# Kernel tuning notes

Hardware: AMD Instinct MI355X
Metric: run time of the kernel (lower is better)

Reference implementation:

```python
import jax, jax.numpy as jnp
import numpy as np

E, E2, T, C, H = 500_000, 1_000_000, 1_000_000, 64, 64
EPS, EPS2 = 0.0, 0.0  # train_eps=False, eps=eps2=0.0


def setup_inputs() -> dict:
    key = jax.random.key(0)
    ks = jax.random.split(key, 16)
    s = 1.0 / np.sqrt(C)
    return {
        "edge_attr": jax.random.normal(ks[0], (E, C), jnp.float32),
        "edge_attr2": jax.random.normal(ks[1], (E2, C), jnp.float32),
        # 6 projection layers (C -> C)
        "Wp": jax.random.normal(ks[2], (6, C, C), jnp.float32) * s,
        "bp": jnp.zeros((6, C), jnp.float32),
        # MLP 0 (for 1-hop edges): C -> H -> C
        "W1a": jax.random.normal(ks[3], (C, H), jnp.float32) * s,
        "b1a": jnp.zeros((H,), jnp.float32),
        "W2a": jax.random.normal(ks[4], (H, C), jnp.float32) * (1.0 / np.sqrt(H)),
        "b2a": jnp.zeros((C,), jnp.float32),
        # MLP 1 (for 2-hop edges): C -> H -> C
        "W1b": jax.random.normal(ks[5], (C, H), jnp.float32) * s,
        "b1b": jnp.zeros((H,), jnp.float32),
        "W2b": jax.random.normal(ks[6], (H, C), jnp.float32) * (1.0 / np.sqrt(H)),
        "b2b": jnp.zeros((C,), jnp.float32),
        # triangle index lists [3, T]; all values < E so valid for both edge arrays
        "triangle_1_1_1": jax.random.randint(ks[7], (3, T), 0, E, jnp.int64),
        "triangle_1_1_2": jax.random.randint(ks[8], (3, T), 0, E, jnp.int64),
        "triangle_1_2_2": jax.random.randint(ks[9], (3, T), 0, E, jnp.int64),
        "triangle_2_2_2": jax.random.randint(ks[10], (3, T), 0, E, jnp.int64),
        "inverse_edge_1": jax.random.randint(ks[11], (E,), 0, E, jnp.int64),
        "inverse_edge_2": jax.random.randint(ks[12], (E2,), 0, E, jnp.int64),
    }


def reference(edge_attr, edge_attr2, Wp, bp, W1a, b1a, W2a, b2a,
              W1b, b1b, W2b, b2b,
              triangle_1_1_1, triangle_1_1_2, triangle_1_2_2, triangle_2_2_2,
              inverse_edge_1, inverse_edge_2):
    num_edges = edge_attr.shape[0]
    num_edges2 = edge_attr2.shape[0]

    def proj(i, x):  # Linear proj i applied to gathered-sum features
        return x @ Wp[i] + bp[i]

    def mlp_a(x):
        return jax.nn.relu(x @ W1a + b1a) @ W2a + b2a

    def mlp_b(x):
        return jax.nn.relu(x @ W1b + b1b) @ W2b + b2b

    ij111, ik111, kj111 = triangle_1_1_1
    ij112, ik112, kj112 = triangle_1_1_2
    ij122, ik122, kj122 = triangle_1_2_2
    ij222, ik222, kj222 = triangle_2_2_2

    m111 = jax.ops.segment_sum(proj(0, edge_attr[ik111] + edge_attr[kj111]), ij111, num_segments=num_edges)
    m112 = jax.ops.segment_sum(proj(1, edge_attr[ik112] + edge_attr2[kj112]), ij112, num_segments=num_edges)
    m122 = jax.ops.segment_sum(proj(2, edge_attr2[ik122] + edge_attr2[kj122]), ij122, num_segments=num_edges)
    edge_attr = mlp_a(edge_attr * (1.0 + EPS) + m111 + m112 + m112[inverse_edge_1] + m122)

    m211 = jax.ops.segment_sum(proj(3, edge_attr[ij112] + edge_attr[ik112]), kj112, num_segments=num_edges2)
    m212 = jax.ops.segment_sum(proj(4, edge_attr[ij122] + edge_attr2[kj122]), ik122, num_segments=num_edges2)
    m222 = jax.ops.segment_sum(proj(5, edge_attr2[ik222] + edge_attr2[kj222]), ij222, num_segments=num_edges2)
    edge_attr2 = mlp_b(edge_attr2 * (1.0 + EPS2) + m211 + m212 + m212[inverse_edge_2] + m222)

    return (edge_attr, edge_attr2)
```

## Files before the change

### kernel.cpp

```cpp
#include <hip/hip_runtime.h>

#define CH 64
typedef unsigned int uint;
typedef unsigned short ushort;

typedef __attribute__((ext_vector_type(8))) short bf16x8;
typedef __attribute__((ext_vector_type(4))) float f32x4;

__device__ __forceinline__ float bf_lo(uint u){ union{uint a;float f;}c; c.a=u<<16; return c.f; }
__device__ __forceinline__ float bf_hi(uint u){ union{uint a;float f;}c; c.a=u&0xffff0000u; return c.f; }
__device__ __forceinline__ ushort f2bf(float f){
    uint a = __float_as_uint(f);
    a = (a + 0x7fffu + ((a>>16)&1u)) >> 16;
    return (ushort)a;
}
__device__ __forceinline__ uint pack2(float lo, float hi){
    return (uint)f2bf(lo) | ((uint)f2bf(hi) << 16);
}
__device__ __forceinline__ void atom_pk(uint* addr, float lo, float hi){
    uint v = pack2(lo, hi);
    asm volatile("global_atomic_pk_add_bf16 %0, %1, off" :: "v"(addr), "v"(v));
}

template<bool ABF, bool BBF>
__global__ __launch_bounds__(256) void scatter_sum(
    const void* __restrict__ Av, const void* __restrict__ Bv,
    const int* __restrict__ idx_dst, const int* __restrict__ idx_a,
    const int* __restrict__ idx_b, int T,
    uint* __restrict__ S, float* __restrict__ cnt)
{
    const int l32  = threadIdx.x & 31;
    const int half = (threadIdx.x >> 5) & 1;
    const int wave  = blockIdx.x * (blockDim.x >> 6) + (threadIdx.x >> 6);
    const int nwave = gridDim.x * (blockDim.x >> 6);

    for (int w = wave; 4 * w < T; w += nwave) {
        const int t0 = 4 * w + half;
        const int t1 = t0 + 2;
        const bool v0 = t0 < T, v1 = t1 < T;
        const int u0 = v0 ? t0 : 0;
        const int u1 = v1 ? t1 : 0;
        const int ia0 = idx_a[u0], ib0 = idx_b[u0], id0 = idx_dst[u0];
        const int ia1 = idx_a[u1], ib1 = idx_b[u1], id1 = idx_dst[u1];

        float ax0, ay0, bx0, by0, ax1, ay1, bx1, by1;
        if (ABF) { uint u = ((const uint*)Av)[(size_t)ia0*32 + l32]; ax0 = bf_lo(u); ay0 = bf_hi(u); }
        else     { float2 v = ((const float2*)Av)[(size_t)ia0*32 + l32]; ax0 = v.x; ay0 = v.y; }
        if (BBF) { uint u = ((const uint*)Bv)[(size_t)ib0*32 + l32]; bx0 = bf_lo(u); by0 = bf_hi(u); }
        else     { float2 v = ((const float2*)Bv)[(size_t)ib0*32 + l32]; bx0 = v.x; by0 = v.y; }
        if (ABF) { uint u = ((const uint*)Av)[(size_t)ia1*32 + l32]; ax1 = bf_lo(u); ay1 = bf_hi(u); }
        else     { float2 v = ((const float2*)Av)[(size_t)ia1*32 + l32]; ax1 = v.x; ay1 = v.y; }
        if (BBF) { uint u = ((const uint*)Bv)[(size_t)ib1*32 + l32]; bx1 = bf_lo(u); by1 = bf_hi(u); }
        else     { float2 v = ((const float2*)Bv)[(size_t)ib1*32 + l32]; bx1 = v.x; by1 = v.y; }

        if (v0) {
            atom_pk(S + (size_t)id0*32 + l32, ax0+bx0, ay0+by0);
            if (l32 == 0) atomicAdd(&cnt[id0], 1.0f);
        }
        if (v1) {
            atom_pk(S + (size_t)id1*32 + l32, ax1+bx1, ay1+by1);
            if (l32 == 0) atomicAdd(&cnt[id1], 1.0f);
        }
    }
}

__global__ __launch_bounds__(256) void conv_bf16_kernel(
    const float* __restrict__ src, uint* __restrict__ dst, long n4)
{
    long i = (long)blockIdx.x * blockDim.x + threadIdx.x;
    const long stride = (long)gridDim.x * blockDim.x;
    for (; i < n4; i += stride) {
        const float4 v = ((const float4*)src)[i];
        uint2 o; o.x = pack2(v.x, v.y); o.y = pack2(v.z, v.w);
        ((uint2*)dst)[i] = o;
    }
}

__global__ __launch_bounds__(256) void fused_finalize_mfma(
    const float* __restrict__ base,
    const uint* __restrict__ SA, const float* __restrict__ cA,
    const float* __restrict__ WA, const float* __restrict__ bA,
    const uint* __restrict__ SB, const float* __restrict__ cB,
    const float* __restrict__ WB, const float* __restrict__ bB,
    const uint* __restrict__ SC, const float* __restrict__ cC,
    const float* __restrict__ WC, const float* __restrict__ bC,
    const int* __restrict__ inv,
    const float* __restrict__ W1, const float* __restrict__ b1,
    const float* __restrict__ W2, const float* __restrict__ b2,
    int N, float* __restrict__ out, uint* __restrict__ out_bf)
{
    __shared__ __attribute__((aligned(16))) char lds[49152];
    const int tid = threadIdx.x;

    const float* Wlist[5] = {WA, WB, WC, W1, W2};
    #pragma unroll
    for (int m = 0; m < 5; ++m) {
        const float* Wm = Wlist[m];
        for (int idx = tid; idx < 4096; idx += 256) {
            const int k = idx >> 6, col = idx & 63;
            *(ushort*)(lds + m*8192 + col*128 + ((2*k) ^ ((col&7)<<4))) = f2bf(Wm[idx]);
        }
    }
    __syncthreads();

    const int w = tid >> 6, lane = tid & 63;
    const int ln = lane & 15, grp = lane >> 4;
    const int r0 = blockIdx.x * 64 + w * 16;
    const int ra = (r0 + ln) < N ? (r0 + ln) : (N - 1);
    const int iva = inv[ra];
    char* zl = lds + 40960 + w * 2048;

    auto ldS = [&](const uint* Srow, int kc) {
        union { uint4 u; bf16x8 h; } c;
        c.u = *(const uint4*)(Srow + kc*16 + grp*4);
        return c.h;
    };
    auto ldS2 = [&](const uint* r1, const uint* r2, int kc) {
        const uint4 a = *(const uint4*)(r1 + kc*16 + grp*4);
        const uint4 b = *(const uint4*)(r2 + kc*16 + grp*4);
        union { uint4 u; bf16x8 h; } c;
        c.u.x = pack2(bf_lo(a.x)+bf_lo(b.x), bf_hi(a.x)+bf_hi(b.x));
        c.u.y = pack2(bf_lo(a.y)+bf_lo(b.y), bf_hi(a.y)+bf_hi(b.y));
        c.u.z = pack2(bf_lo(a.z)+bf_lo(b.z), bf_hi(a.z)+bf_hi(b.z));
        c.u.w = pack2(bf_lo(a.w)+bf_lo(b.w), bf_hi(a.w)+bf_hi(b.w));
        return c.h;
    };
    auto ldW = [&](int m, int kc, int ct) {
        const int col = ct*16 + ln;
        const int k2  = (kc*32 + grp*8) * 2;
        return *(const bf16x8*)(lds + m*8192 + col*128 + (k2 ^ ((col&7)<<4)));
    };
    auto ldZ = [&](int kc) {
        const int k2 = (kc*32 + grp*8) * 2;
        return *(const bf16x8*)(zl + ln*128 + (k2 ^ ((ln&7)<<4)));
    };
    auto stZ = [&](int row, int col, float v) {
        *(ushort*)(zl + row*128 + ((2*col) ^ ((row&7)<<4))) = f2bf(v);
    };

    const uint* SArow  = SA + (size_t)ra * 32;
    const uint* SBrow  = SB + (size_t)ra * 32;
    const uint* SCrow  = SC + (size_t)ra * 32;
    const uint* SCrow2 = SC + (size_t)iva * 32;

    const f32x4 z4 = {0.f, 0.f, 0.f, 0.f};
    f32x4 acc[4] = {z4, z4, z4, z4};

    #pragma unroll
    for (int kc = 0; kc < 2; ++kc) {
        const bf16x8 aA = ldS(SArow, kc);
        const bf16x8 aB = ldS(SBrow, kc);
        const bf16x8 aC = ldS2(SCrow, SCrow2, kc);
        #pragma unroll
        for (int ct = 0; ct < 4; ++ct) {
            acc[ct] = __builtin_amdgcn_mfma_f32_16x16x32_bf16(aA, ldW(0,kc,ct), acc[ct], 0,0,0);
            acc[ct] = __builtin_amdgcn_mfma_f32_16x16x32_bf16(aB, ldW(1,kc,ct), acc[ct], 0,0,0);
            acc[ct] = __builtin_amdgcn_mfma_f32_16x16x32_bf16(aC, ldW(2,kc,ct), acc[ct], 0,0,0);
        }
    }

    #pragma unroll
    for (int reg = 0; reg < 4; ++reg) {
        const int rd = r0 + grp*4 + reg;
        const int rc = rd < N ? rd : (N - 1);
        const float fA = cA[rc], fB = cB[rc];
        const float fC = cC[rc] + cC[inv[rc]];
        #pragma unroll
        for (int ct = 0; ct < 4; ++ct) {
            const int col = ct*16 + ln;
            acc[ct][reg] += base[(size_t)rc*64 + col] + fA*bA[col] + fB*bB[col] + fC*bC[col];
        }
    }
    #pragma unroll
    for (int ct = 0; ct < 4; ++ct)
        #pragma unroll
        for (int reg = 0; reg < 4; ++reg)
            stZ(grp*4 + reg, ct*16 + ln, acc[ct][reg]);

    f32x4 hacc[4] = {z4, z4, z4, z4};
    #pragma unroll
    for (int kc = 0; kc < 2; ++kc) {
        const bf16x8 az = ldZ(kc);
        #pragma unroll
        for (int ct = 0; ct < 4; ++ct)
            hacc[ct] = __builtin_amdgcn_mfma_f32_16x16x32_bf16(az, ldW(3,kc,ct), hacc[ct], 0,0,0);
    }
    #pragma unroll
    for (int ct = 0; ct < 4; ++ct)
        #pragma unroll
        for (int reg = 0; reg < 4; ++reg)
            stZ(grp*4 + reg, ct*16 + ln, fmaxf(hacc[ct][reg] + b1[ct*16 + ln], 0.f));

    f32x4 oacc[4] = {z4, z4, z4, z4};
    #pragma unroll
    for (int kc = 0; kc < 2; ++kc) {
        const bf16x8 ah = ldZ(kc);
        #pragma unroll
        for (int ct = 0; ct < 4; ++ct)
            oacc[ct] = __builtin_amdgcn_mfma_f32_16x16x32_bf16(ah, ldW(4,kc,ct), oacc[ct], 0,0,0);
    }
    #pragma unroll
    for (int reg = 0; reg < 4; ++reg) {
        const int rd = r0 + grp*4 + reg;
        if (rd < N) {
            #pragma unroll
            for (int ct = 0; ct < 4; ++ct) {
                const int col = ct*16 + ln;
                const float o = oacc[ct][reg] + b2[col];
                out[(size_t)rd*64 + col] = o;
                if (out_bf) ((ushort*)out_bf)[(size_t)rd*64 + col] = f2bf(o);
            }
        }
    }
}

extern "C" void kernel_launch(void* const* d_in, const int* in_sizes, int n_in,
                              void* d_out, int out_size, void* d_ws, size_t ws_size,
                              hipStream_t stream)
{
    const float* ea  = (const float*)d_in[0];
    const float* ea2 = (const float*)d_in[1];
    const float* Wp  = (const float*)d_in[2];
    const float* bp  = (const float*)d_in[3];
    const float* W1a = (const float*)d_in[4];
    const float* b1a = (const float*)d_in[5];
    const float* W2a = (const float*)d_in[6];
    const float* b2a = (const float*)d_in[7];
    const float* W1b = (const float*)d_in[8];
    const float* b1b = (const float*)d_in[9];
    const float* W2b = (const float*)d_in[10];
    const float* b2b = (const float*)d_in[11];
    const int* t111 = (const int*)d_in[12];
    const int* t112 = (const int*)d_in[13];
    const int* t122 = (const int*)d_in[14];
    const int* t222 = (const int*)d_in[15];
    const int* inv1 = (const int*)d_in[16];
    const int* inv2 = (const int*)d_in[17];

    const int E    = in_sizes[0] / CH;
    const int E2   = in_sizes[1] / CH;
    const int T111 = in_sizes[12] / 3;
    const int T112 = in_sizes[13] / 3;
    const int T122 = in_sizes[14] / 3;
    const int T222 = in_sizes[15] / 3;

    float* out1 = (float*)d_out;
    float* out2 = out1 + (size_t)E * CH;

    const size_t R = (size_t)(E > E2 ? E : E2);
    char* p = (char*)d_ws;
    uint*  SA = (uint*)p;  p += R * 128;
    uint*  SB = (uint*)p;  p += R * 128;
    uint*  SC = (uint*)p;  p += R * 128;
    float* cA = (float*)p; p += R * 4;
    float* cB = (float*)p; p += R * 4;
    float* cC = (float*)p; p += R * 4;
    size_t used = (size_t)(p - (char*)d_ws);
    uint* ea2_bf = nullptr;
    uint* out1_bf = nullptr;
    uint* ea_bf  = nullptr;
    if (ws_size >= used + (size_t)E2 * 128) { ea2_bf = (uint*)p; p += (size_t)E2 * 128; used += (size_t)E2 * 128; }
    if (ws_size >= used + (size_t)E  * 128) { out1_bf = (uint*)p; p += (size_t)E * 128; used += (size_t)E * 128; }
    if (ws_size >= used + (size_t)E  * 128) { ea_bf  = (uint*)p; }

    const dim3 blk256(256);
    const int SCAT_NB = 4096;

    auto scat = [&](const void* A, bool abf, const void* B, bool bbf,
                    const int* dst, const int* ia, const int* ib, int T,
                    uint* S, float* c) {
        if (abf && bbf)
            scatter_sum<true, true ><<<SCAT_NB, blk256, 0, stream>>>(A, B, dst, ia, ib, T, S, c);
        else if (abf)
            scatter_sum<true, false><<<SCAT_NB, blk256, 0, stream>>>(A, B, dst, ia, ib, T, S, c);
        else if (bbf)
            scatter_sum<false, true><<<SCAT_NB, blk256, 0, stream>>>(A, B, dst, ia, ib, T, S, c);
        else
            scatter_sum<false, false><<<SCAT_NB, blk256, 0, stream>>>(A, B, dst, ia, ib, T, S, c);
    };

    if (ea2_bf) conv_bf16_kernel<<<2048, blk256, 0, stream>>>(ea2, ea2_bf, (long)E2 * 16);
    if (ea_bf)  conv_bf16_kernel<<<2048, blk256, 0, stream>>>(ea,  ea_bf,  (long)E  * 16);

    const void* eaS  = ea_bf  ? (const void*)ea_bf  : (const void*)ea;
    const void* ea2S = ea2_bf ? (const void*)ea2_bf : (const void*)ea2;
    const bool eaB = ea_bf != nullptr, ea2B = ea2_bf != nullptr;

    hipMemsetAsync(SA, 0, (size_t)E * 128, stream);
    hipMemsetAsync(SB, 0, (size_t)E * 128, stream);
    hipMemsetAsync(SC, 0, (size_t)E * 128, stream);
    hipMemsetAsync(cA, 0, (size_t)E * 4, stream);
    hipMemsetAsync(cB, 0, (size_t)E * 4, stream);
    hipMemsetAsync(cC, 0, (size_t)E * 4, stream);

    scat(eaS, eaB, eaS, eaB, t111 + 0, t111 + T111, t111 + 2*T111, T111, SA, cA);
    scat(ea2S, ea2B, ea2S, ea2B, t122 + 0, t122 + T122, t122 + 2*T122, T122, SB, cB);
    scat(eaS, eaB, ea2S, ea2B, t112 + 0, t112 + T112, t112 + 2*T112, T112, SC, cC);

    fused_finalize_mfma<<<(E + 63) / 64, blk256, 0, stream>>>(
        ea,
        SA, cA, Wp + 0*CH*CH, bp + 0*CH,
        SB, cB, Wp + 2*CH*CH, bp + 2*CH,
        SC, cC, Wp + 1*CH*CH, bp + 1*CH,
        inv1, W1a, b1a, W2a, b2a, E, out1, out1_bf);

    hipMemsetAsync(SA, 0, (size_t)E2 * 128, stream);
    hipMemsetAsync(SB, 0, (size_t)E2 * 128, stream);
    hipMemsetAsync(SC, 0, (size_t)E2 * 128, stream);
    hipMemsetAsync(cA, 0, (size_t)E2 * 4, stream);
    hipMemsetAsync(cB, 0, (size_t)E2 * 4, stream);
    hipMemsetAsync(cC, 0, (size_t)E2 * 4, stream);

    const void* o1S = out1_bf ? (const void*)out1_bf : (const void*)out1;
    const bool o1B = out1_bf != nullptr;

    scat(o1S, o1B, o1S, o1B, t112 + 2*T112, t112 + 0, t112 + T112, T112, SA, cA);
    scat(ea2S, ea2B, ea2S, ea2B, t222 + 0, t222 + T222, t222 + 2*T222, T222, SB, cB);
    scat(o1S, o1B, ea2S, ea2B, t122 + T122, t122 + 0, t122 + 2*T122, T122, SC, cC);

    fused_finalize_mfma<<<(E2 + 63) / 64, blk256, 0, stream>>>(
        ea2,
        SA, cA, Wp + 3*CH*CH, bp + 3*CH,
        SB, cB, Wp + 5*CH*CH, bp + 5*CH,
        SC, cC, Wp + 4*CH*CH, bp + 4*CH,
        inv2, W1b, b1b, W2b, b2b, E2, out2, nullptr);
}
```

Baseline: 1.642 ms.

## Merge three scatter launches into one multi-job kernel with deeper per-wave batching

Replaces three sequential scatter_sum launches per stage with a single scatter3_deep launch that splits the grid into three job partitions running at the same time. Each half-wave now handles four triangles per iteration instead of two, so more gathers are in flight before the atomics. The scatter buffers are made contiguous so each stage zeroes them with two memsets instead of six. The intent is to cut launch overhead and tail idling and to raise memory-level parallelism. In exchange, the bf16/fp32 flags become runtime branches rather than template parameters, and the kernel needs more registers.

New measurement: 1.604 ms. -2.3%, faster.

```diff
diff --git a/kernel.cpp b/kernel.cpp
--- a/kernel.cpp
+++ b/kernel.cpp
@@ -22,44 +22,55 @@
     asm volatile("global_atomic_pk_add_bf16 %0, %1, off" :: "v"(addr), "v"(v));
 }
 
-template<bool ABF, bool BBF>
-__global__ __launch_bounds__(256) void scatter_sum(
-    const void* __restrict__ Av, const void* __restrict__ Bv,
-    const int* __restrict__ idx_dst, const int* __restrict__ idx_a,
-    const int* __restrict__ idx_b, int T,
-    uint* __restrict__ S, float* __restrict__ cnt)
+struct SJob {
+    const void* A; const void* B;
+    const int* dst; const int* ia; const int* ib;
+    uint* S; float* cnt;
+    int T; int abf; int bbf;
+};
+struct SJobs { SJob j[3]; };
+
+__global__ __launch_bounds__(256) void scatter3_deep(SJobs JJ)
 {
+    const int nbj = gridDim.x / 3;
+    int job = blockIdx.x / nbj; if (job > 2) job = 2;
+    const int nb = (job == 2) ? (gridDim.x - 2 * nbj) : nbj;
+    const int bj = blockIdx.x - job * nbj;
+
+    const SJob J = JJ.j[job];
     const int l32  = threadIdx.x & 31;
     const int half = (threadIdx.x >> 5) & 1;
-    const int wave  = blockIdx.x * (blockDim.x >> 6) + (threadIdx.x >> 6);
-    const int nwave = gridDim.x * (blockDim.x >> 6);
-
-    for (int w = wave; 4 * w < T; w += nwave) {
-        const int t0 = 4 * w + half;
-        const int t1 = t0 + 2;
-        const bool v0 = t0 < T, v1 = t1 < T;
-        const int u0 = v0 ? t0 : 0;
-        const int u1 = v1 ? t1 : 0;
-        const int ia0 = idx_a[u0], ib0 = idx_b[u0], id0 = idx_dst[u0];
-        const int ia1 = idx_a[u1], ib1 = idx_b[u1], id1 = idx_dst[u1];
-
-        float ax0, ay0, bx0, by0, ax1, ay1, bx1, by1;
-        if (ABF) { uint u = ((const uint*)Av)[(size_t)ia0*32 + l32]; ax0 = bf_lo(u); ay0 = bf_hi(u); }
-        else     { float2 v = ((const float2*)Av)[(size_t)ia0*32 + l32]; ax0 = v.x; ay0 = v.y; }
-        if (BBF) { uint u = ((const uint*)Bv)[(size_t)ib0*32 + l32]; bx0 = bf_lo(u); by0 = bf_hi(u); }
-        else     { float2 v = ((const float2*)Bv)[(size_t)ib0*32 + l32]; bx0 = v.x; by0 = v.y; }
-        if (ABF) { uint u = ((const uint*)Av)[(size_t)ia1*32 + l32]; ax1 = bf_lo(u); ay1 = bf_hi(u); }
-        else     { float2 v = ((const float2*)Av)[(size_t)ia1*32 + l32]; ax1 = v.x; ay1 = v.y; }
-        if (BBF) { uint u = ((const uint*)Bv)[(size_t)ib1*32 + l32]; bx1 = bf_lo(u); by1 = bf_hi(u); }
-        else     { float2 v = ((const float2*)Bv)[(size_t)ib1*32 + l32]; bx1 = v.x; by1 = v.y; }
-
-        if (v0) {
-            atom_pk(S + (size_t)id0*32 + l32, ax0+bx0, ay0+by0);
-            if (l32 == 0) atomicAdd(&cnt[id0], 1.0f);
-        }
-        if (v1) {
-            atom_pk(S + (size_t)id1*32 + l32, ax1+bx1, ay1+by1);
-            if (l32 == 0) atomicAdd(&cnt[id1], 1.0f);
+    const int wave  = bj * 4 + (threadIdx.x >> 6);
+    const int nwave = nb * 4;
+    const bool abf = J.abf != 0, bbf = J.bbf != 0;
+    const int T = J.T;
+
+    for (int t0 = wave * 8 + half * 4; t0 < T; t0 += nwave * 8) {
+        int idd[4], iaa[4], ibb[4]; bool v[4];
+        #pragma unroll
+        for (int k = 0; k < 4; ++k) {
+            const int t = t0 + k;
+            v[k] = t < T;
+            const int u = v[k] ? t : 0;
+            iaa[k] = J.ia[u]; ibb[k] = J.ib[u]; idd[k] = J.dst[u];
+        }
+        float ax[4], ay[4], bx[4], by[4];
+        #pragma unroll
+        for (int k = 0; k < 4; ++k) {
+            if (abf) { uint u = ((const uint*)J.A)[(size_t)iaa[k]*32 + l32]; ax[k]=bf_lo(u); ay[k]=bf_hi(u); }
+            else     { float2 f = ((const float2*)J.A)[(size_t)iaa[k]*32 + l32]; ax[k]=f.x; ay[k]=f.y; }
+        }
+        #pragma unroll
+        for (int k = 0; k < 4; ++k) {
+            if (bbf) { uint u = ((const uint*)J.B)[(size_t)ibb[k]*32 + l32]; bx[k]=bf_lo(u); by[k]=bf_hi(u); }
+            else     { float2 f = ((const float2*)J.B)[(size_t)ibb[k]*32 + l32]; bx[k]=f.x; by[k]=f.y; }
+        }
+        #pragma unroll
+        for (int k = 0; k < 4; ++k) {
+            if (v[k]) {
+                atom_pk(J.S + (size_t)idd[k]*32 + l32, ax[k]+bx[k], ay[k]+by[k]);
+                if (l32 == 0) atomicAdd(&J.cnt[idd[k]], 1.0f);
+            }
         }
     }
 }
@@ -249,12 +260,8 @@
 
     const size_t R = (size_t)(E > E2 ? E : E2);
     char* p = (char*)d_ws;
-    uint*  SA = (uint*)p;  p += R * 128;
-    uint*  SB = (uint*)p;  p += R * 128;
-    uint*  SC = (uint*)p;  p += R * 128;
-    float* cA = (float*)p; p += R * 4;
-    float* cB = (float*)p; p += R * 4;
-    float* cC = (float*)p; p += R * 4;
+    uint*  Sbase = (uint*)p;  p += 3 * R * 128;
+    float* cbase = (float*)p; p += 3 * R * 4;
     size_t used = (size_t)(p - (char*)d_ws);
     uint* ea2_bf = nullptr;
     uint* out1_bf = nullptr;
@@ -266,62 +273,53 @@
     const dim3 blk256(256);
     const int SCAT_NB = 4096;
 
-    auto scat = [&](const void* A, bool abf, const void* B, bool bbf,
-                    const int* dst, const int* ia, const int* ib, int T,
-                    uint* S, float* c) {
-        if (abf && bbf)
-            scatter_sum<true, true ><<<SCAT_NB, blk256, 0, stream>>>(A, B, dst, ia, ib, T, S, c);
-        else if (abf)
-            scatter_sum<true, false><<<SCAT_NB, blk256, 0, stream>>>(A, B, dst, ia, ib, T, S, c);
-        else if (bbf)
-            scatter_sum<false, true><<<SCAT_NB, blk256, 0, stream>>>(A, B, dst, ia, ib, T, S, c);
-        else
-            scatter_sum<false, false><<<SCAT_NB, blk256, 0, stream>>>(A, B, dst, ia, ib, T, S, c);
-    };
-
     if (ea2_bf) conv_bf16_kernel<<<2048, blk256, 0, stream>>>(ea2, ea2_bf, (long)E2 * 16);
     if (ea_bf)  conv_bf16_kernel<<<2048, blk256, 0, stream>>>(ea,  ea_bf,  (long)E  * 16);
 
     const void* eaS  = ea_bf  ? (const void*)ea_bf  : (const void*)ea;
     const void* ea2S = ea2_bf ? (const void*)ea2_bf : (const void*)ea2;
-    const bool eaB = ea_bf != nullptr, ea2B = ea2_bf != nullptr;
-
-    hipMemsetAsync(SA, 0, (size_t)E * 128, stream);
-    hipMemsetAsync(SB, 0, (size_t)E * 128, stream);
-    hipMemsetAsync(SC, 0, (size_t)E * 128, stream);
-    hipMemsetAsync(cA, 0, (size_t)E * 4, stream);
-    hipMemsetAsync(cB, 0, (size_t)E * 4, stream);
-    hipMemsetAsync(cC, 0, (size_t)E * 4, stream);
-
-    scat(eaS, eaB, eaS, eaB, t111 + 0, t111 + T111, t111 + 2*T111, T111, SA, cA);
-    scat(ea2S, ea2B, ea2S, ea2B, t122 + 0, t122 + T122, t122 + 2*T122, T122, SB, cB);
-    scat(eaS, eaB, ea2S, ea2B, t112 + 0, t112 + T112, t112 + 2*T112, T112, SC, cC);
+    const int eaB = ea_bf != nullptr, ea2B = ea2_bf != nullptr;
+
+    uint*  SA1 = Sbase;              uint*  SB1 = Sbase + (size_t)E * 32;  uint*  SC1 = Sbase + (size_t)2*E * 32;
+    float* cA1 = cbase;              float* cB1 = cbase + E;               float* cC1 = cbase + (size_t)2*E;
+    hipMemsetAsync(Sbase, 0, (size_t)3 * E * 128, stream);
+    hipMemsetAsync(cbase, 0, (size_t)3 * E * 4, stream);
+
+    {
+        SJobs J;
+        J.j[0] = {eaS,  eaS,  t111 + 0, t111 + T111, t111 + 2*T111, SA1, cA1, T111, eaB,  eaB};
+        J.j[1] = {ea2S, ea2S, t122 + 0, t122 + T122, t122 + 2*T122, SB1, cB1, T122, ea2B, ea2B};
+        J.j[2] = {eaS,  ea2S, t112 + 0, t112 + T112, t112 + 2*T112, SC1, cC1, T112, eaB,  ea2B};
+        scatter3_deep<<<SCAT_NB, blk256, 0, stream>>>(J);
+    }
 
     fused_finalize_mfma<<<(E + 63) / 64, blk256, 0, stream>>>(
         ea,
-        SA, cA, Wp + 0*CH*CH, bp + 0*CH,
-        SB, cB, Wp + 2*CH*CH, bp + 2*CH,
-        SC, cC, Wp + 1*CH*CH, bp + 1*CH,
+        SA1, cA1, Wp + 0*CH*CH, bp + 0*CH,
+        SB1, cB1, Wp + 2*CH*CH, bp + 2*CH,
+        SC1, cC1, Wp + 1*CH*CH, bp + 1*CH,
         inv1, W1a, b1a, W2a, b2a, E, out1, out1_bf);
 
-    hipMemsetAsync(SA, 0, (size_t)E2 * 128, stream);
-    hipMemsetAsync(SB, 0, (size_t)E2 * 128, stream);
-    hipMemsetAsync(SC, 0, (size_t)E2 * 128, stream);
-    hipMemsetAsync(cA, 0, (size_t)E2 * 4, stream);
-    hipMemsetAsync(cB, 0, (size_t)E2 * 4, stream);
-    hipMemsetAsync(cC, 0, (size_t)E2 * 4, stream);
+    uint*  SA2 = Sbase;              uint*  SB2 = Sbase + (size_t)E2 * 32; uint*  SC2 = Sbase + (size_t)2*E2 * 32;
+    float* cA2 = cbase;              float* cB2 = cbase + E2;              float* cC2 = cbase + (size_t)2*E2;
+    hipMemsetAsync(Sbase, 0, (size_t)3 * E2 * 128, stream);
+    hipMemsetAsync(cbase, 0, (size_t)3 * E2 * 4, stream);
 
     const void* o1S = out1_bf ? (const void*)out1_bf : (const void*)out1;
-    const bool o1B = out1_bf != nullptr;
-
-    scat(o1S, o1B, o1S, o1B, t112 + 2*T112, t112 + 0, t112 + T112, T112, SA, cA);
-    scat(ea2S, ea2B, ea2S, ea2B, t222 + 0, t222 + T222, t222 + 2*T222, T222, SB, cB);
-    scat(o1S, o1B, ea2S, ea2B, t122 + T122, t122 + 0, t122 + 2*T122, T122, SC, cC);
+    const int o1B = out1_bf != nullptr;
+
+    {
+        SJobs J;
+        J.j[0] = {o1S,  o1S,  t112 + 2*T112, t112 + 0, t112 + T112,   SA2, cA2, T112, o1B,  o1B};
+        J.j[1] = {ea2S, ea2S, t222 + 0,      t222 + T222, t222 + 2*T222, SB2, cB2, T222, ea2B, ea2B};
+        J.j[2] = {o1S,  ea2S, t122 + T122,   t122 + 0, t122 + 2*T122, SC2, cC2, T122, o1B,  ea2B};
+        scatter3_deep<<<SCAT_NB, blk256, 0, stream>>>(J);
+    }
 
     fused_finalize_mfma<<<(E2 + 63) / 64, blk256, 0, stream>>>(
         ea2,
-        SA, cA, Wp + 3*CH*CH, bp + 3*CH,
-        SB, cB, Wp + 5*CH*CH, bp + 5*CH,
-        SC, cC, Wp + 4*CH*CH, bp + 4*CH,
+        SA2, cA2, Wp + 3*CH*CH, bp + 3*CH,
+        SB2, cB2, Wp + 5*CH*CH, bp + 5*CH,
+        SC2, cC2, Wp + 4*CH*CH, bp + 4*CH,
         inv2, W1b, b1b, W2b, b2b, E2, out2, nullptr);
 }
```
